# Performance work log

Hardware: AMD Instinct MI355X
Metric: run time of the kernel (lower is better)

## Reference

```python
import jax, jax.numpy as jnp
import numpy as np

H = 64  # LSTM units for both layers
T = 128  # sequence length
D = 128  # input feature dim
B = 2048  # batch

def setup_inputs() -> dict:
    key = jax.random.key(0)
    ks = jax.random.split(key, 7)
    s_in = 1.0 / np.sqrt(D)
    s_h = 1.0 / np.sqrt(H)
    return {
        "x": jax.random.normal(ks[0], (B, T, D), dtype=jnp.float32),
        # Keras LSTM weights: kernel [in, 4H], recurrent_kernel [H, 4H], bias [4H]
        # gate order: i, f, g (cell candidate), o
        "W1": jax.random.normal(ks[1], (D, 4 * H), dtype=jnp.float32) * s_in,
        "U1": jax.random.normal(ks[2], (H, 4 * H), dtype=jnp.float32) * s_h,
        "b1": jnp.zeros((4 * H,), dtype=jnp.float32),
        "W2": jax.random.normal(ks[3], (H, 4 * H), dtype=jnp.float32) * s_h,
        "U2": jax.random.normal(ks[4], (H, 4 * H), dtype=jnp.float32) * s_h,
        "b2": jnp.zeros((4 * H,), dtype=jnp.float32),
    }

def _lstm(x, W, U, b, act):
    """Keras-faithful LSTM, return_sequences=True, zero init state.
    x: [B, T, D_in] -> hs: [B, T, H]
    recurrent_activation = sigmoid; `act` is the cell/output activation.
    """
    Bsz = x.shape[0]
    # Precompute input projections for all timesteps (one big GEMM).
    xz = jnp.einsum('btd,dg->btg', x, W) + b  # [B, T, 4H]
    xz = jnp.swapaxes(xz, 0, 1)  # [T, B, 4H]

    def step(carry, zt):
        h, c = carry
        z = zt + h @ U  # [B, 4H]
        i, f, g, o = jnp.split(z, 4, axis=-1)
        i = jax.nn.sigmoid(i)
        f = jax.nn.sigmoid(f)
        g = act(g)
        o = jax.nn.sigmoid(o)
        c = f * c + i * g
        h = o * act(c)
        return (h, c), h

    init = (jnp.zeros((Bsz, H), x.dtype), jnp.zeros((Bsz, H), x.dtype))
    _, hs = jax.lax.scan(step, init, xz)  # hs: [T, B, H]
    return jnp.swapaxes(hs, 0, 1)  # [B, T, H]

def reference(x, W1, U1, b1, W2, U2, b2):
    h1 = _lstm(x, W1, U1, b1, jnp.tanh)           # layer 1: default tanh
    h2 = _lstm(h1, W2, U2, b2, jax.nn.sigmoid)    # layer 2: activation='sigmoid'
    return h2.reshape(h2.shape[0], T * H, 1)      # Reshape((8192, 1))
```

## Files before the change

kernel.cpp:

```cpp
#include <hip/hip_runtime.h>
#include <stdint.h>

typedef __attribute__((ext_vector_type(8))) short short8;
typedef __attribute__((ext_vector_type(4))) short short4_t;
typedef __attribute__((ext_vector_type(4))) float floatx4;

#define TT 128
#define DD 128

#define BARRIER_LDS() asm volatile("s_waitcnt lgkmcnt(0)\n\ts_barrier" ::: "memory")

__device__ __forceinline__ short f2bf(float f) {
  union { float f; uint32_t u; } v; v.f = f;
  uint32_t u = v.u;
  u += 0x7fffu + ((u >> 16) & 1u);
  return (short)(u >> 16);
}

__device__ __forceinline__ float sigf(float x) {
  return __builtin_amdgcn_rcpf(1.f + __expf(-x));
}
__device__ __forceinline__ float tanhf_(float x) {
  return 2.f * __builtin_amdgcn_rcpf(1.f + __expf(-2.f * x)) - 1.f;
}

__global__ void wtrans_all(const float* __restrict__ W1, const float* __restrict__ U1,
                           const float* __restrict__ W2, const float* __restrict__ U2,
                           short* __restrict__ w1t, short* __restrict__ u1t,
                           short* __restrict__ w2t, short* __restrict__ u2t) {
  int n = blockIdx.x;
  int k = threadIdx.x;
  w1t[n * 128 + k] = f2bf(W1[k * 256 + n]);
  if (k < 64) {
    u1t[n * 64 + k] = f2bf(U1[k * 256 + n]);
    w2t[n * 64 + k] = f2bf(W2[k * 256 + n]);
    u2t[n * 64 + k] = f2bf(U2[k * 256 + n]);
  }
}

__global__ __launch_bounds__(512, 2) void lstm_fused(
    const float* __restrict__ x,
    const short* __restrict__ w1t, const short* __restrict__ u1t,
    const short* __restrict__ w2t, const short* __restrict__ u2t,
    const float* __restrict__ b1, const float* __restrict__ b2,
    float* __restrict__ out) {
  __shared__ short hb1[2][8 * 80];
  __shared__ short hb2[2][8 * 80];
  __shared__ short xbuf[2][8 * 144];

  const int tid = threadIdx.x;
  const int w = tid >> 6;
  const bool isL1 = (w < 4);
  const int wg = w & 3;
  const int lane = tid & 63;
  const int mrow = lane & 15;
  const int quad = lane >> 4;
  const int rowbase = blockIdx.x * 8;
  const int colw = wg * 16 + mrow;
  const int br_a = 2 * (mrow >> 2) + (mrow & 1);

  short8 wA[4][4], uA[4][2];
  float bias[4];
  if (isL1) {
#pragma unroll
    for (int g = 0; g < 4; ++g) {
      const int n = g * 4 + wg;
#pragma unroll
      for (int s = 0; s < 4; ++s)
        wA[g][s] = *(const short8*)(w1t + n * 2048 + mrow * 128 + quad * 8 + s * 32);
#pragma unroll
      for (int s = 0; s < 2; ++s)
        uA[g][s] = *(const short8*)(u1t + n * 1024 + mrow * 64 + quad * 8 + s * 32);
      bias[g] = b1[g * 64 + colw];
    }
  } else {
#pragma unroll
    for (int g = 0; g < 4; ++g) {
      const int n = g * 4 + wg;
#pragma unroll
      for (int s = 0; s < 2; ++s) {
        wA[g][s]     = *(const short8*)(w2t + n * 1024 + mrow * 64 + quad * 8 + s * 32);
        wA[g][2 + s] = *(const short8*)(u2t + n * 1024 + mrow * 64 + quad * 8 + s * 32);
      }
      bias[g] = b2[g * 64 + colw];
    }
  }

  const int tid2 = tid & 255;
  const int sxr = tid2 >> 5;
  const int sxc = (tid2 & 31) * 4;
  const float* xload = x + (size_t)(rowbase + sxr) * (TT * DD) + sxc;

  short8 h1f[2], xh[4];
#pragma unroll
  for (int s = 0; s < 2; ++s)
#pragma unroll
    for (int j = 0; j < 8; ++j) h1f[s][j] = 0;
#pragma unroll
  for (int s = 0; s < 4; ++s)
#pragma unroll
    for (int j = 0; j < 8; ++j) xh[s][j] = 0;
  float cc[2] = {0.f, 0.f};
  floatx4 xnext;

  for (int idx = tid; idx < 2 * 8 * 80; idx += 512) ((short*)hb2)[idx] = 0;
  if (!isL1) {
    floatx4 x0 = *(const floatx4*)xload;
    short4_t v;
#pragma unroll
    for (int j = 0; j < 4; ++j) v[j] = f2bf(x0[j]);
    *(short4_t*)&xbuf[0][sxr * 144 + sxc] = v;
    xnext = *(const floatx4*)(xload + DD);
  }
  BARRIER_LDS();
  if (isL1) {
#pragma unroll
    for (int s = 0; s < 4; ++s)
      xh[s] = *(const short8*)&xbuf[0][br_a * 144 + (quad + 4 * s) * 8];
  }

  float* outp = out + (size_t)rowbase * 8192 + colw;

#pragma unroll 1
  for (int i = 0; i <= TT; ++i) {
    const int p = i & 1;

    if (isL1) {
      if (i < TT) {
        floatx4 acc[4];
#pragma unroll
        for (int g = 0; g < 4; ++g) acc[g] = floatx4{0.f, 0.f, 0.f, 0.f};
#pragma unroll
        for (int g = 0; g < 4; ++g) {
#pragma unroll
          for (int s = 0; s < 4; ++s)
            acc[g] = __builtin_amdgcn_mfma_f32_16x16x32_bf16(xh[s], wA[g][s], acc[g], 0, 0, 0);
#pragma unroll
          for (int s = 0; s < 2; ++s)
            acc[g] = __builtin_amdgcn_mfma_f32_16x16x32_bf16(h1f[s], uA[g][s], acc[g], 0, 0, 0);
        }
#pragma unroll
        for (int r = 0; r < 2; ++r) {
          float ig = sigf(acc[0][r] + bias[0]);
          float fg = sigf(acc[1][r] + bias[1]);
          float gg = tanhf_(acc[2][r] + bias[2]);
          float og = sigf(acc[3][r] + bias[3]);
          float c = fg * cc[r] + ig * gg;
          cc[r] = c;
          float h = og * tanhf_(c);
          hb1[p][(2 * quad + r) * 80 + colw] = f2bf(h);
        }
      }
    } else {
      {
        short4_t v;
#pragma unroll
        for (int j = 0; j < 4; ++j) v[j] = f2bf(xnext[j]);
        *(short4_t*)&xbuf[1 - p][sxr * 144 + sxc] = v;
        int tn = (i + 2 < TT) ? i + 2 : TT - 1;
        xnext = *(const floatx4*)(xload + (size_t)tn * DD);
      }
      if (i >= 1) {
        floatx4 acc[4];
#pragma unroll
        for (int g = 0; g < 4; ++g) acc[g] = floatx4{0.f, 0.f, 0.f, 0.f};
#pragma unroll
        for (int g = 0; g < 4; ++g) {
#pragma unroll
          for (int s = 0; s < 2; ++s)
            acc[g] = __builtin_amdgcn_mfma_f32_16x16x32_bf16(h1f[s], wA[g][s], acc[g], 0, 0, 0);
#pragma unroll
          for (int s = 0; s < 2; ++s)
            acc[g] = __builtin_amdgcn_mfma_f32_16x16x32_bf16(xh[s], wA[g][2 + s], acc[g], 0, 0, 0);
        }
#pragma unroll
        for (int r = 0; r < 2; ++r) {
          float ig = sigf(acc[0][r] + bias[0]);
          float fg = sigf(acc[1][r] + bias[1]);
          float gg = sigf(acc[2][r] + bias[2]);
          float og = sigf(acc[3][r] + bias[3]);
          float c = fg * cc[r] + ig * gg;
          cc[r] = c;
          float h = og * sigf(c);
          hb2[p][(2 * quad + r) * 80 + colw] = f2bf(h);
          outp[(size_t)(2 * quad + r) * 8192 + (i - 1) * 64] = h;
        }
      }
    }

    BARRIER_LDS();

    if (i < TT) {
      if (isL1) {
#pragma unroll
        for (int s = 0; s < 2; ++s)
          h1f[s] = *(const short8*)&hb1[p][br_a * 80 + (quad + 4 * s) * 8];
#pragma unroll
        for (int s = 0; s < 4; ++s)
          xh[s] = *(const short8*)&xbuf[1 - p][br_a * 144 + (quad + 4 * s) * 8];
      } else {
#pragma unroll
        for (int s = 0; s < 2; ++s) {
          h1f[s] = *(const short8*)&hb1[p][br_a * 80 + (quad + 4 * s) * 8];
          xh[s]  = *(const short8*)&hb2[p][br_a * 80 + (quad + 4 * s) * 8];
        }
      }
    }
  }
}

extern "C" void kernel_launch(void* const* d_in, const int* in_sizes, int n_in,
                              void* d_out, int out_size, void* d_ws, size_t ws_size,
                              hipStream_t stream) {
  const float* x  = (const float*)d_in[0];
  const float* W1 = (const float*)d_in[1];
  const float* U1 = (const float*)d_in[2];
  const float* b1 = (const float*)d_in[3];
  const float* W2 = (const float*)d_in[4];
  const float* U2 = (const float*)d_in[5];
  const float* b2 = (const float*)d_in[6];
  float* out = (float*)d_out;

  short* w1t = (short*)d_ws;
  short* u1t = w1t + 32768;
  short* w2t = u1t + 16384;
  short* u2t = w2t + 16384;

  hipLaunchKernelGGL(wtrans_all, dim3(256), dim3(128), 0, stream,
                     W1, U1, W2, U2, w1t, u1t, w2t, u2t);
  hipLaunchKernelGGL(lstm_fused, dim3(256), dim3(512), 0, stream,
                     x, w1t, u1t, w2t, u2t, b1, b2, out);
}
```

Before: 287.4 us.

## Move LDS fragment loads into step body, interleave MFMA gates, deepen x prefetch

Fragment reads from LDS (h1, h2 and x) now happen at the top of each step, reading the buffer written in the previous step, rather than after the barrier. Zero-initialised hb1 replaces the register zeroing. The MFMA loops are reordered so the four independent gate accumulators alternate, which hides MFMA dependency latency. The layer-2 waves prefetch x two steps ahead and do the conversion and LDS store after issuing their MFMAs, so the global load and conversion overlap with matrix work. The cost is one more live float4 register and a change in how LDS reads line up with the barrier.

After: 327.7 us. 14.0% more time.

```diff
diff --git a/kernel.cpp b/kernel.cpp
--- a/kernel.cpp
+++ b/kernel.cpp
@@ -92,32 +92,23 @@
   const float* xload = x + (size_t)(rowbase + sxr) * (TT * DD) + sxc;
 
   short8 h1f[2], xh[4];
-#pragma unroll
-  for (int s = 0; s < 2; ++s)
-#pragma unroll
-    for (int j = 0; j < 8; ++j) h1f[s][j] = 0;
-#pragma unroll
-  for (int s = 0; s < 4; ++s)
-#pragma unroll
-    for (int j = 0; j < 8; ++j) xh[s][j] = 0;
   float cc[2] = {0.f, 0.f};
-  floatx4 xnext;
-
-  for (int idx = tid; idx < 2 * 8 * 80; idx += 512) ((short*)hb2)[idx] = 0;
+  floatx4 xcur, xnxt;
+
+  for (int idx = tid; idx < 2 * 8 * 80; idx += 512) {
+    ((short*)hb1)[idx] = 0;
+    ((short*)hb2)[idx] = 0;
+  }
   if (!isL1) {
     floatx4 x0 = *(const floatx4*)xload;
     short4_t v;
 #pragma unroll
     for (int j = 0; j < 4; ++j) v[j] = f2bf(x0[j]);
     *(short4_t*)&xbuf[0][sxr * 144 + sxc] = v;
-    xnext = *(const floatx4*)(xload + DD);
+    xcur = *(const floatx4*)(xload + DD);
+    xnxt = *(const floatx4*)(xload + 2 * DD);
   }
   BARRIER_LDS();
-  if (isL1) {
-#pragma unroll
-    for (int s = 0; s < 4; ++s)
-      xh[s] = *(const short8*)&xbuf[0][br_a * 144 + (quad + 4 * s) * 8];
-  }
 
   float* outp = out + (size_t)rowbase * 8192 + colw;
 
@@ -127,18 +118,26 @@
 
     if (isL1) {
       if (i < TT) {
+#pragma unroll
+        for (int s = 0; s < 4; ++s)
+          xh[s] = *(const short8*)&xbuf[p][br_a * 144 + (quad + 4 * s) * 8];
+        h1f[0] = *(const short8*)&hb1[1 - p][br_a * 80 + quad * 8];
+        h1f[1] = *(const short8*)&hb1[1 - p][br_a * 80 + (quad + 4) * 8];
+
         floatx4 acc[4];
 #pragma unroll
         for (int g = 0; g < 4; ++g) acc[g] = floatx4{0.f, 0.f, 0.f, 0.f};
 #pragma unroll
-        for (int g = 0; g < 4; ++g) {
-#pragma unroll
-          for (int s = 0; s < 4; ++s)
+        for (int s = 0; s < 4; ++s)
+#pragma unroll
+          for (int g = 0; g < 4; ++g)
             acc[g] = __builtin_amdgcn_mfma_f32_16x16x32_bf16(xh[s], wA[g][s], acc[g], 0, 0, 0);
 #pragma unroll
-          for (int s = 0; s < 2; ++s)
+        for (int s = 0; s < 2; ++s)
+#pragma unroll
+          for (int g = 0; g < 4; ++g)
             acc[g] = __builtin_amdgcn_mfma_f32_16x16x32_bf16(h1f[s], uA[g][s], acc[g], 0, 0, 0);
-        }
+
 #pragma unroll
         for (int r = 0; r < 2; ++r) {
           float ig = sigf(acc[0][r] + bias[0]);
@@ -152,27 +151,37 @@
         }
       }
     } else {
-      {
-        short4_t v;
-#pragma unroll
-        for (int j = 0; j < 4; ++j) v[j] = f2bf(xnext[j]);
-        *(short4_t*)&xbuf[1 - p][sxr * 144 + sxc] = v;
-        int tn = (i + 2 < TT) ? i + 2 : TT - 1;
-        xnext = *(const floatx4*)(xload + (size_t)tn * DD);
-      }
       if (i >= 1) {
+        h1f[0] = *(const short8*)&hb1[1 - p][br_a * 80 + quad * 8];
+        h1f[1] = *(const short8*)&hb1[1 - p][br_a * 80 + (quad + 4) * 8];
+        xh[0]  = *(const short8*)&hb2[1 - p][br_a * 80 + quad * 8];
+        xh[1]  = *(const short8*)&hb2[1 - p][br_a * 80 + (quad + 4) * 8];
+
         floatx4 acc[4];
 #pragma unroll
         for (int g = 0; g < 4; ++g) acc[g] = floatx4{0.f, 0.f, 0.f, 0.f};
 #pragma unroll
-        for (int g = 0; g < 4; ++g) {
-#pragma unroll
-          for (int s = 0; s < 2; ++s)
+        for (int s = 0; s < 2; ++s)
+#pragma unroll
+          for (int g = 0; g < 4; ++g)
             acc[g] = __builtin_amdgcn_mfma_f32_16x16x32_bf16(h1f[s], wA[g][s], acc[g], 0, 0, 0);
 #pragma unroll
-          for (int s = 0; s < 2; ++s)
+        for (int s = 0; s < 2; ++s)
+#pragma unroll
+          for (int g = 0; g < 4; ++g)
             acc[g] = __builtin_amdgcn_mfma_f32_16x16x32_bf16(xh[s], wA[g][2 + s], acc[g], 0, 0, 0);
+
+        if (i <= TT - 2) {
+          short4_t v;
+#pragma unroll
+          for (int j = 0; j < 4; ++j) v[j] = f2bf(xcur[j]);
+          *(short4_t*)&xbuf[1 - p][sxr * 144 + sxc] = v;
+          xcur = xnxt;
+          const int tn = (i + 3 < TT) ? (i + 3) : (TT - 1);
+          xnxt = *(const floatx4*)(xload + (size_t)tn * DD);
         }
+
+        const int t = i - 1;
 #pragma unroll
         for (int r = 0; r < 2; ++r) {
           float ig = sigf(acc[0][r] + bias[0]);
@@ -183,29 +192,19 @@
           cc[r] = c;
           float h = og * sigf(c);
           hb2[p][(2 * quad + r) * 80 + colw] = f2bf(h);
-          outp[(size_t)(2 * quad + r) * 8192 + (i - 1) * 64] = h;
+          outp[(size_t)(2 * quad + r) * 8192 + t * 64] = h;
         }
+      } else {
+        short4_t v;
+#pragma unroll
+        for (int j = 0; j < 4; ++j) v[j] = f2bf(xcur[j]);
+        *(short4_t*)&xbuf[1 - p][sxr * 144 + sxc] = v;
+        xcur = xnxt;
+        xnxt = *(const floatx4*)(xload + (size_t)3 * DD);
       }
     }
 
     BARRIER_LDS();
-
-    if (i < TT) {
-      if (isL1) {
-#pragma unroll
-        for (int s = 0; s < 2; ++s)
-          h1f[s] = *(const short8*)&hb1[p][br_a * 80 + (quad + 4 * s) * 8];
-#pragma unroll
-        for (int s = 0; s < 4; ++s)
-          xh[s] = *(const short8*)&xbuf[1 - p][br_a * 144 + (quad + 4 * s) * 8];
-      } else {
-#pragma unroll
-        for (int s = 0; s < 2; ++s) {
-          h1f[s] = *(const short8*)&hb1[p][br_a * 80 + (quad + 4 * s) * 8];
-          xh[s]  = *(const short8*)&hb2[p][br_a * 80 + (quad + 4 * s) * 8];
-        }
-      }
-    }
   }
 }
 
```
